# Kernel tuning notes

Hardware: AMD Instinct MI355X
Metric: run time of the kernel (lower is better)

## Reference

```python
import jax, jax.numpy as jnp
import numpy as np

B, L, D = 4, 2048, 2048
H, KVH, HD = 16, 4, 128          # num_heads, num_kv_heads, head_dim = D // H
M = 16                           # mem_tokens
BASE = 10000.0
EPS = 1.1920929e-07              # torch F.rms_norm default eps = fp32 machine eps


def _rms_norm(x):
    # normalize over last dim, no learned weight (matches F.rms_norm(x, (hd,)))
    return x * jax.lax.rsqrt(jnp.mean(x * x, axis=-1, keepdims=True) + EPS)


def _apply_rotary(x, cos, sin):
    # x: [B, h, T, HD]; cos/sin: [1, 1, T, HD//2]
    half = x.shape[-1] // 2
    x1, x2 = x[..., :half], x[..., half:]
    return jnp.concatenate([x1 * cos + x2 * sin, -x1 * sin + x2 * cos], axis=-1)


def setup_inputs() -> dict:
    key = jax.random.key(0)
    k0, k1, k2, k3, k4 = jax.random.split(key, 5)
    kv_dim = KVH * HD
    s = 0.02
    return {
        "x": jax.random.normal(k0, (B, L, D), dtype=jnp.float32),
        "Wq": jax.random.normal(k1, (D, D), dtype=jnp.float32) * s,
        "Wk": jax.random.normal(k2, (kv_dim, D), dtype=jnp.float32) * s,
        "Wv": jax.random.normal(k3, (kv_dim, D), dtype=jnp.float32) * s,
        "Wproj": jax.random.normal(k4, (D, D), dtype=jnp.float32) * s,
        "q_gain": jnp.full((H,), 1.0, dtype=jnp.float32),
    }


def reference(x, Wq, Wk, Wv, Wproj, q_gain):
    Bx, Lx, Dx = x.shape
    # QKV projections (Linear: x @ W.T), split into heads -> [B, h, L, HD]
    q = (x @ Wq.T).reshape(Bx, Lx, H, HD).transpose(0, 2, 1, 3)
    k = (x @ Wk.T).reshape(Bx, Lx, KVH, HD).transpose(0, 2, 1, 3)
    v = (x @ Wv.T).reshape(Bx, Lx, KVH, HD).transpose(0, 2, 1, 3)
    # QK RMSNorm
    q = _rms_norm(q)
    k = _rms_norm(k)
    # RoPE on the non-memory tokens only
    T = Lx - M
    inv_freq = 1.0 / BASE ** (jnp.arange(0, HD, 2, dtype=jnp.float32) / HD)
    freqs = jnp.outer(jnp.arange(T, dtype=jnp.float32), inv_freq)  # [T, HD//2]
    cos = jnp.cos(freqs)[None, None]
    sin = jnp.sin(freqs)[None, None]
    q = jnp.concatenate([q[:, :, :M], _apply_rotary(q[:, :, M:], cos, sin)], axis=2)
    k = jnp.concatenate([k[:, :, :M], _apply_rotary(k[:, :, M:], cos, sin)], axis=2)
    # per-head gain on q
    q = q * q_gain[None, :, None, None]
    # GQA attention: group q heads by kv head (matches repeat_interleave ordering)
    rep = H // KVH
    qg = q.reshape(Bx, KVH, rep, Lx, HD)
    scale = 1.0 / np.sqrt(HD).astype(np.float32)
    scores = jnp.einsum('bgrqd,bgkd->bgrqk', qg, k) * scale  # [B, KVH, rep, L, L]
    causal = jnp.tril(jnp.ones((Lx, Lx), dtype=bool))
    scores = jnp.where(causal, scores, -jnp.inf)
    p = jax.nn.softmax(scores, axis=-1)
    y = jnp.einsum('bgrqk,bgkd->bgrqd', p, v)                # [B, KVH, rep, L, HD]
    y = y.reshape(Bx, H, Lx, HD).transpose(0, 2, 1, 3).reshape(Bx, Lx, Dx)
    return y @ Wproj.T
```

## Files before the change

kernel.cpp:

```cpp
#include <hip/hip_runtime.h>
#include <stdint.h>

typedef unsigned short u16;
typedef short s8v __attribute__((ext_vector_type(8)));
typedef float f4v __attribute__((ext_vector_type(4)));
typedef float f16v __attribute__((ext_vector_type(16)));

typedef __attribute__((address_space(1))) char gchar;
typedef __attribute__((address_space(3))) char lchar;

static __device__ __forceinline__ u16 f2bf(float f) {
  uint32_t x = __float_as_uint(f);
  x += 0x7fffu + ((x >> 16) & 1u);
  return (u16)(x >> 16);
}
static __device__ __forceinline__ float bf2f(u16 u) {
  return __uint_as_float(((uint32_t)u) << 16);
}
static __device__ __forceinline__ void gload_lds16(const void* g, void* l) {
  __builtin_amdgcn_global_load_lds((gchar*)(uintptr_t)g,
                                   (lchar*)(uint32_t)(uintptr_t)l, 16, 0, 0);
}

__global__ __launch_bounds__(256) void cvt_bf16(const float4* __restrict__ src,
                                                uint2* __restrict__ dst, int n4) {
  int i = blockIdx.x * 256 + threadIdx.x;
  int st = gridDim.x * 256;
  for (; i < n4; i += st) {
    float4 v = src[i];
    uint2 o;
    o.x = (uint32_t)f2bf(v.x) | ((uint32_t)f2bf(v.y) << 16);
    o.y = (uint32_t)f2bf(v.z) | ((uint32_t)f2bf(v.w) << 16);
    dst[i] = o;
  }
}

__global__ __launch_bounds__(256) void cvt_bf16_w(const float4* __restrict__ s0,
                                                  const float4* __restrict__ s1,
                                                  const float4* __restrict__ s2,
                                                  const float4* __restrict__ s3,
                                                  uint2* __restrict__ dst) {
  int i = blockIdx.x * 256 + threadIdx.x;
  int st = gridDim.x * 256;
  for (; i < 2621440; i += st) {
    const float4* s;
    int off;
    if (i < 1048576)      { s = s0; off = i; }
    else if (i < 1310720) { s = s1; off = i - 1048576; }
    else if (i < 1572864) { s = s2; off = i - 1310720; }
    else                  { s = s3; off = i - 1572864; }
    float4 v = s[off];
    uint2 o;
    o.x = (uint32_t)f2bf(v.x) | ((uint32_t)f2bf(v.y) << 16);
    o.y = (uint32_t)f2bf(v.z) | ((uint32_t)f2bf(v.w) << 16);
    dst[i] = o;
  }
}

__global__ __launch_bounds__(256) void rope_table(float* __restrict__ tc,
                                                  float* __restrict__ ts) {
  int i = blockIdx.x * 256 + threadIdx.x;
  if (i >= 2032 * 64) return;
  int t = i >> 6, f = i & 63;
  float invf = 1.0f / powf(10000.0f, (float)f * (1.0f / 64.0f));
  float ang = (float)t * invf;
  float s, c;
  sincosf(ang, &s, &c);
  tc[i] = c;
  ts[i] = s;
}

template <int BN, int OUT>
__global__ __launch_bounds__(512, 2) void gemm_nt(
    const u16* __restrict__ A, const u16* __restrict__ Wt,
    u16* __restrict__ Oa, u16* __restrict__ Ob2, float* __restrict__ OF) {
  constexpr int MI = (BN == 256) ? 8 : 4;
  constexpr int BLOADS = (BN == 256) ? 2 : 1;
  __shared__ u16 lA[2][2][256 * 32];
  __shared__ u16 lB[2][2][BN * 32];
  const int tid = threadIdx.x;
  const int lane = tid & 63, wid = tid >> 6;
  const int wr = (BN == 256) ? (wid >> 2) : (wid >> 1);
  const int wc = (BN == 256) ? (wid & 3) : (wid & 1);
  const int l15 = lane & 15, l4 = lane >> 4;

  const int bid = blockIdx.x;
  const int swz = (bid & 7) * 32 + (bid >> 3);
  const int bn = swz >> 5, bm = swz & 31;
  const int m0 = bm * 256;
  const int n0r = bn * BN;

  auto stage_part = [&](int kt, int bs, int ks) {
    const int kb = kt * 64 + ks * 32;
#pragma unroll
    for (int c = 0; c < 2; ++c) {
      int cidx = tid + c * 512;
      int r = cidx >> 2, q = cidx & 3;
      int cc = q ^ ((r >> 2) & 3);
      gload_lds16(A + (size_t)(m0 + r) * 2048 + kb + cc * 8,
                  &lA[bs][ks][cidx * 8]);
    }
#pragma unroll
    for (int c = 0; c < BLOADS; ++c) {
      int cidx = tid + c * 512;
      int r = cidx >> 2, q = cidx & 3;
      int cc = q ^ ((r >> 2) & 3);
      gload_lds16(Wt + (size_t)(n0r + r) * 2048 + kb + cc * 8,
                  &lB[bs][ks][cidx * 8]);
    }
  };
  auto roff = [&](int fr, int c) {
    return (fr * 4 + (c ^ ((fr >> 2) & 3))) * 8;
  };

  const f4v Z4 = {0.f, 0.f, 0.f, 0.f};
  f4v acc[MI][4];
#pragma unroll
  for (int i = 0; i < MI; i++)
#pragma unroll
    for (int j = 0; j < 4; j++) acc[i][j] = Z4;

  stage_part(0, 0, 0); stage_part(0, 0, 1);
  stage_part(1, 1, 0); stage_part(1, 1, 1);

  const int NT = 32;
  for (int t = 0; t < NT; ++t) {
    const int bs = t & 1;
    if (t + 1 < NT) {
      if constexpr (BN == 256) asm volatile("s_waitcnt vmcnt(8)" ::: "memory");
      else                     asm volatile("s_waitcnt vmcnt(6)" ::: "memory");
    } else {
      asm volatile("s_waitcnt vmcnt(0)" ::: "memory");
    }
    asm volatile("s_barrier" ::: "memory");
    const bool pf = (t + 2 < NT);
#pragma unroll
    for (int ks = 0; ks < 2; ++ks) {
      s8v afrg[MI], bfrg[4];
#pragma unroll
      for (int i = 0; i < MI; ++i)
        afrg[i] = *(const s8v*)&lA[bs][ks][roff(wr * (MI * 16) + i * 16 + l15, l4)];
#pragma unroll
      for (int j = 0; j < 4; ++j)
        bfrg[j] = *(const s8v*)&lB[bs][ks][roff(wc * 64 + j * 16 + l15, l4)];
      asm volatile("s_waitcnt lgkmcnt(0)" ::: "memory");
      __builtin_amdgcn_sched_barrier(0);
      asm volatile("s_barrier" ::: "memory");
      if (pf) stage_part(t + 2, bs, ks);
      __builtin_amdgcn_s_setprio(1);
#pragma unroll
      for (int i = 0; i < MI; ++i)
#pragma unroll
        for (int j = 0; j < 4; ++j)
          acc[i][j] = __builtin_amdgcn_mfma_f32_16x16x32_bf16(afrg[i], bfrg[j], acc[i][j], 0, 0, 0);
      __builtin_amdgcn_s_setprio(0);
    }
  }

  const int colg = bn * BN + wc * 64;
  if constexpr (OUT == 0) {
    const int hh = colg >> 7, d0 = colg & 127;
#pragma unroll
    for (int i = 0; i < MI; i++)
#pragma unroll
      for (int r = 0; r < 4; r++) {
        int m = m0 + wr * (MI * 16) + i * 16 + l4 * 4 + r;
        int b = m >> 11, l = m & 2047;
        size_t base = ((size_t)(b * 16 + hh) * 2048 + l) * 128 + d0;
#pragma unroll
        for (int j = 0; j < 4; j++)
          Oa[base + j * 16 + l15] = f2bf(acc[i][j][r]);
      }
  } else if constexpr (OUT == 1) {
    u16* Ob = (colg < 512) ? Oa : Ob2;
    const int hh = (colg & 511) >> 7, d0 = colg & 127;
#pragma unroll
    for (int i = 0; i < MI; i++)
#pragma unroll
      for (int r = 0; r < 4; r++) {
        int m = m0 + wr * (MI * 16) + i * 16 + l4 * 4 + r;
        int b = m >> 11, l = m & 2047;
        size_t base = ((size_t)(b * 4 + hh) * 2048 + l) * 128 + d0;
#pragma unroll
        for (int j = 0; j < 4; j++)
          Ob[base + j * 16 + l15] = f2bf(acc[i][j][r]);
      }
  } else {
#pragma unroll
    for (int i = 0; i < MI; i++)
#pragma unroll
      for (int r = 0; r < 4; r++) {
        int m = m0 + wr * (MI * 16) + i * 16 + l4 * 4 + r;
#pragma unroll
        for (int j = 0; j < 4; j++)
          OF[(size_t)m * 2048 + colg + j * 16 + l15] = acc[i][j][r];
      }
  }
}

__global__ __launch_bounds__(256) void norm_rope(u16* __restrict__ buf,
                                                 const float* __restrict__ gain,
                                                 const float* __restrict__ tc,
                                                 const float* __restrict__ ts) {
  const int lane = threadIdx.x & 63;
  const int gw = blockIdx.x * 4 + (threadIdx.x >> 6);
  const int nw = gridDim.x * 4;
  for (int row = gw; row < 163840; row += nw) {
    int l = row & 2047;
    u16* p = buf + (size_t)row * 128;
    float x1 = bf2f(p[lane]);
    float x2 = bf2f(p[lane + 64]);
    float ss = x1 * x1 + x2 * x2;
#pragma unroll
    for (int off = 32; off > 0; off >>= 1) ss += __shfl_xor(ss, off, 64);
    float r = rsqrtf(ss * (1.0f / 128.0f) + 1.1920929e-07f);
    x1 *= r; x2 *= r;
    if (l >= 16) {
      int t = l - 16;
      float c = tc[t * 64 + lane], s = ts[t * 64 + lane];
      float o1 = x1 * c + x2 * s;
      float o2 = -x1 * s + x2 * c;
      x1 = o1; x2 = o2;
    }
    if (row < 131072) {
      float g = gain[(row >> 11) & 15] *
                (0.08838834764831845f * 1.4426950408889634f);
      x1 *= g; x2 *= g;
    }
    p[lane] = f2bf(x1);
    p[lane + 64] = f2bf(x2);
  }
}

__global__ __launch_bounds__(256) void transpose_v(const u16* __restrict__ v,
                                                   u16* __restrict__ vt) {
  __shared__ u16 t[64][64];
  const int l0 = blockIdx.x * 64, d0 = blockIdx.y * 64, bg = blockIdx.z;
  const int tid = threadIdx.x;
#pragma unroll
  for (int it = 0; it < 2; ++it) {
    int lin = it * 256 + tid;
    int r = lin >> 3, cb = lin & 7;
    s8v val = *(const s8v*)&v[((bg * 2048 + l0 + r) * 128) + d0 + cb * 8];
    *(s8v*)&t[r][(cb ^ (r & 7)) * 8] = val;
  }
  __syncthreads();
#pragma unroll
  for (int it = 0; it < 2; ++it) {
    int lin = it * 256 + tid;
    int r2 = lin >> 3, c2 = (lin & 7) * 8;
    s8v o;
#pragma unroll
    for (int j = 0; j < 8; ++j) {
      int rr = c2 + j, cc = r2;
      o[j] = (short)t[rr][(cc & 7) + 8 * ((cc >> 3) ^ (rr & 7))];
    }
    *(s8v*)&vt[((bg * 128 + d0 + r2) * 2048) + l0 + c2] = o;
  }
}

__global__ __launch_bounds__(256, 2) void attn(const u16* __restrict__ q,
                                               const u16* __restrict__ k,
                                               const u16* __restrict__ vt,
                                               u16* __restrict__ y) {
  __shared__ u16 lK[2][64 * 128];
  __shared__ u16 lVT[2][128 * 64];
  const int tid = threadIdx.x;
  const int lane = tid & 63, wid = tid >> 6;
  const int l31 = lane & 31, hi = lane >> 5;

  const int db = (int)blockIdx.y * 32 + (int)blockIdx.x;
  const int half = db >> 8, rem = db & 255;
  const int bg = (rem & 7) + 8 * half;
  const int pairi = rem >> 3;
  const int b = bg >> 2, g = bg & 3;
  const int h = g * 4 + wid;

  const u16* qh = q + (size_t)(b * 16 + h) * 2048 * 128;
  const u16* kb0 = k + (size_t)(b * 4 + g) * 2048 * 128;
  const u16* vtb0 = vt + (size_t)(b * 4 + g) * 128 * 2048;

  auto stage = [&](int t, int bufsel) {
    const int kv0 = t * 64;
#pragma unroll
    for (int it = 0; it < 4; ++it) {
      int lin = it * 256 + tid;
      int kj = lin >> 4, s = lin & 15;
      gload_lds16(kb0 + (size_t)(kv0 + kj) * 128 + ((s ^ (kj & 7)) * 8),
                  &lK[bufsel][lin * 8]);
    }
#pragma unroll
    for (int it = 0; it < 4; ++it) {
      int lin = it * 256 + tid;
      int d = lin >> 3, s = lin & 7;
      gload_lds16(vtb0 + (size_t)d * 2048 + kv0 + ((s ^ (d & 7)) * 8),
                  &lVT[bufsel][lin * 8]);
    }
  };

  for (int ph = 0; ph < 2; ++ph) {
    const int qt = ph ? (63 - pairi) : pairi;
    const int q0 = qt * 32;
    const int nt = (q0 >> 6) + 1;
    const int qabs = q0 + l31;

    s8v qf[8];
#pragma unroll
    for (int ks = 0; ks < 8; ++ks)
      qf[ks] = *(const s8v*)&qh[(q0 + l31) * 128 + ks * 16 + hi * 8];

    f16v yacc[4];
#pragma unroll
    for (int j = 0; j < 4; ++j)
#pragma unroll
      for (int r = 0; r < 16; ++r) yacc[j][r] = 0.f;
    float mrow = -1e30f, lrow = 0.f;

    stage(0, 0);
    __syncthreads();

    for (int t = 0; t < nt; ++t) {
      const int cur = t & 1;
      if (t + 1 < nt) stage(t + 1, cur ^ 1);
      const int kv0 = t * 64;

      f16v s0a, s1a;
#pragma unroll
      for (int r = 0; r < 16; ++r) { s0a[r] = 0.f; s1a[r] = 0.f; }
      __builtin_amdgcn_s_setprio(1);
#pragma unroll
      for (int ks = 0; ks < 8; ++ks) {
        const int slot = (2 * ks + hi) ^ (l31 & 7);
        s8v kf0 = *(const s8v*)&lK[cur][(l31)*128 + slot * 8];
        s8v kf1 = *(const s8v*)&lK[cur][(32 + l31) * 128 + slot * 8];
        s0a = __builtin_amdgcn_mfma_f32_32x32x16_bf16(kf0, qf[ks], s0a, 0, 0, 0);
        s1a = __builtin_amdgcn_mfma_f32_32x32x16_bf16(kf1, qf[ks], s1a, 0, 0, 0);
      }
      __builtin_amdgcn_s_setprio(0);

      const bool last = (t == nt - 1);
      float p0[16], p1[16];
      float pmax = -1e30f;
#pragma unroll
      for (int r = 0; r < 16; ++r) {
        const int kvloc = (r & 3) + 8 * (r >> 2) + 4 * hi;
        float v0 = s0a[r];
        float v1 = s1a[r];
        if (last) {
          if (kv0 + kvloc > qabs) v0 = -1e30f;
          if (kv0 + 32 + kvloc > qabs) v1 = -1e30f;
        }
        p0[r] = v0; p1[r] = v1;
        pmax = fmaxf(pmax, fmaxf(v0, v1));
      }
      pmax = fmaxf(pmax, __shfl_xor(pmax, 32, 64));

      if (!__all(pmax - mrow <= 11.541560327111707f)) {
        float mnew = fmaxf(mrow, pmax);
        float corr = __builtin_amdgcn_exp2f(mrow - mnew);
#pragma unroll
        for (int r = 0; r < 16; ++r) {
          const int qloc = (r & 3) + 8 * (r >> 2) + 4 * hi;
          float cb = __shfl(corr, qloc, 64);
          yacc[0][r] *= cb; yacc[1][r] *= cb; yacc[2][r] *= cb; yacc[3][r] *= cb;
        }
        lrow *= corr;
        mrow = mnew;
      }

      float ps = 0.f;
#pragma unroll
      for (int r = 0; r < 16; ++r) {
        float e0 = __builtin_amdgcn_exp2f(p0[r] - mrow);
        float e1 = __builtin_amdgcn_exp2f(p1[r] - mrow);
        p0[r] = e0; p1[r] = e1;
        ps += e0 + e1;
      }
      ps += __shfl_xor(ps, 32, 64);
      lrow += ps;

      __builtin_amdgcn_s_setprio(1);
#pragma unroll
      for (int ks = 0; ks < 4; ++ks) {
        const float* pc = (ks < 2) ? p0 : p1;
        const int rb = 8 * (ks & 1);
        uint32_t A0, A1, B0, B1;
        asm("v_cvt_pk_bf16_f32 %0, %1, %2" : "=v"(A0) : "v"(pc[rb + 0]), "v"(pc[rb + 1]));
        asm("v_cvt_pk_bf16_f32 %0, %1, %2" : "=v"(A1) : "v"(pc[rb + 2]), "v"(pc[rb + 3]));
        asm("v_cvt_pk_bf16_f32 %0, %1, %2" : "=v"(B0) : "v"(pc[rb + 4]), "v"(pc[rb + 5]));
        asm("v_cvt_pk_bf16_f32 %0, %1, %2" : "=v"(B1) : "v"(pc[rb + 6]), "v"(pc[rb + 7]));
        uint32_t t0 = hi ? A0 : B0;
        uint32_t t1 = hi ? A1 : B1;
        uint32_t r0 = (uint32_t)__shfl_xor((int)t0, 32, 64);
        uint32_t r1 = (uint32_t)__shfl_xor((int)t1, 32, 64);
        union { uint32_t u[4]; s8v v; } uu;
        uu.u[0] = hi ? r0 : A0;
        uu.u[1] = hi ? r1 : A1;
        uu.u[2] = hi ? B0 : r0;
        uu.u[3] = hi ? B1 : r1;
#pragma unroll
        for (int jd = 0; jd < 4; ++jd) {
          const int rowd = 32 * jd + l31;
          const int slot = (2 * ks + hi) ^ (l31 & 7);
          s8v vf = *(const s8v*)&lVT[cur][rowd * 64 + slot * 8];
          yacc[jd] = __builtin_amdgcn_mfma_f32_32x32x16_bf16(uu.v, vf, yacc[jd], 0, 0, 0);
        }
      }
      __builtin_amdgcn_s_setprio(0);
      __syncthreads();
    }

    float inv = 1.0f / lrow;
#pragma unroll
    for (int r = 0; r < 16; ++r) {
      const int qloc = (r & 3) + 8 * (r >> 2) + 4 * hi;
      float ib = __shfl(inv, qloc, 64);
      const int qrow = q0 + qloc;
      size_t base = ((size_t)(b * 2048 + qrow)) * 2048 + h * 128 + l31;
#pragma unroll
      for (int jd = 0; jd < 4; ++jd)
        y[base + 32 * jd] = f2bf(yacc[jd][r] * ib);
    }
  }
}

extern "C" void kernel_launch(void* const* d_in, const int* in_sizes, int n_in,
                              void* d_out, int out_size, void* d_ws, size_t ws_size,
                              hipStream_t stream) {
  const float* x  = (const float*)d_in[0];
  const float* Wq = (const float*)d_in[1];
  const float* Wk = (const float*)d_in[2];
  const float* Wv = (const float*)d_in[3];
  const float* Wp = (const float*)d_in[4];
  const float* qg = (const float*)d_in[5];
  float* out = (float*)d_out;

  char* ws = (char*)d_ws;
  size_t off = 0;
  auto alloc = [&](size_t bytes) {
    void* p = ws + off;
    off += (bytes + 255) & ~(size_t)255;
    return p;
  };
  u16* x_bf  = (u16*)alloc((size_t)8192 * 2048 * 2);
  u16* wq_bf = (u16*)alloc((size_t)2048 * 2048 * 2);
  u16* wk_bf = (u16*)alloc((size_t)512 * 2048 * 2);
  u16* wv_bf = (u16*)alloc((size_t)512 * 2048 * 2);
  u16* wp_bf = (u16*)alloc((size_t)2048 * 2048 * 2);
  u16* q_bf  = (u16*)alloc((size_t)4 * 16 * 2048 * 128 * 2);
  u16* k_bf  = (u16*)alloc((size_t)4 * 4 * 2048 * 128 * 2);
  u16* v_bf  = (u16*)alloc((size_t)4 * 4 * 2048 * 128 * 2);
  float* tab = (float*)alloc((size_t)2032 * 64 * 2 * 4);
  u16* y_bf  = x_bf;
  u16* vt_bf = wq_bf;

  cvt_bf16<<<2048, 256, 0, stream>>>((const float4*)x, (uint2*)x_bf, 8192 * 2048 / 4);
  cvt_bf16_w<<<1024, 256, 0, stream>>>((const float4*)Wq, (const float4*)Wk,
                                       (const float4*)Wv, (const float4*)Wp,
                                       (uint2*)wq_bf);
  rope_table<<<(2032 * 64 + 255) / 256, 256, 0, stream>>>(tab, tab + 2032 * 64);

  gemm_nt<256, 0><<<dim3(256), 512, 0, stream>>>(x_bf, wq_bf, q_bf, nullptr, nullptr);
  gemm_nt<128, 1><<<dim3(256), 512, 0, stream>>>(x_bf, wk_bf, k_bf, v_bf, nullptr);
  norm_rope<<<2048, 256, 0, stream>>>(q_bf, qg, tab, tab + 2032 * 64);
  transpose_v<<<dim3(32, 2, 16), 256, 0, stream>>>(v_bf, vt_bf);
  attn<<<dim3(32, 16), 256, 0, stream>>>(q_bf, k_bf, vt_bf, y_bf);
  gemm_nt<256, 2><<<dim3(256), 512, 0, stream>>>(y_bf, wp_bf, nullptr, nullptr, out);
}
```

Measured before the change: 357.1 us.

## Fuse Q RMSNorm/RoPE/gain into attention and widen blocks to 512 threads

The Q normalization, rotary embedding and gain scaling move into the attention kernel's Q-fragment load, so the separate norm pass now handles only K and the Q buffer is no longer read and rewritten. The attention kernel switches from a 256-thread block processing two paired 32-row Q tiles in sequence to a 512-thread block processing one 64-row Q tile, with two wave sets sharing each K/V stage. The lane-swap shuffle is replaced by v_permlane32_swap. This trades the causal load balance of paired tiles, since blocks now have uneven work, and adds register pressure under launch_bounds(512,2).

```diff
diff --git a/kernel.cpp b/kernel.cpp
--- a/kernel.cpp
+++ b/kernel.cpp
@@ -198,14 +198,13 @@
   }
 }
 
-__global__ __launch_bounds__(256) void norm_rope(u16* __restrict__ buf,
-                                                 const float* __restrict__ gain,
-                                                 const float* __restrict__ tc,
-                                                 const float* __restrict__ ts) {
+__global__ __launch_bounds__(256) void norm_rope_k(u16* __restrict__ buf,
+                                                   const float* __restrict__ tc,
+                                                   const float* __restrict__ ts) {
   const int lane = threadIdx.x & 63;
   const int gw = blockIdx.x * 4 + (threadIdx.x >> 6);
   const int nw = gridDim.x * 4;
-  for (int row = gw; row < 163840; row += nw) {
+  for (int row = gw; row < 32768; row += nw) {
     int l = row & 2047;
     u16* p = buf + (size_t)row * 128;
     float x1 = bf2f(p[lane]);
@@ -222,11 +221,6 @@
       float o2 = -x1 * s + x2 * c;
       x1 = o1; x2 = o2;
     }
-    if (row < 131072) {
-      float g = gain[(row >> 11) & 15] *
-                (0.08838834764831845f * 1.4426950408889634f);
-      x1 *= g; x2 *= g;
-    }
     p[lane] = f2bf(x1);
     p[lane + 64] = f2bf(x2);
   }
@@ -259,10 +253,13 @@
   }
 }
 
-__global__ __launch_bounds__(256, 2) void attn(const u16* __restrict__ q,
+__global__ __launch_bounds__(512, 2) void attn(const u16* __restrict__ q,
                                                const u16* __restrict__ k,
                                                const u16* __restrict__ vt,
-                                               u16* __restrict__ y) {
+                                               u16* __restrict__ y,
+                                               const float* __restrict__ qg,
+                                               const float* __restrict__ tc,
+                                               const float* __restrict__ ts) {
   __shared__ u16 lK[2][64 * 128];
   __shared__ u16 lVT[2][128 * 64];
   const int tid = threadIdx.x;
@@ -272,155 +269,198 @@
   const int db = (int)blockIdx.y * 32 + (int)blockIdx.x;
   const int half = db >> 8, rem = db & 255;
   const int bg = (rem & 7) + 8 * half;
-  const int pairi = rem >> 3;
+  const int qi = rem >> 3;
+  const int qt = 31 - qi;
   const int b = bg >> 2, g = bg & 3;
-  const int h = g * 4 + wid;
+  const int h = g * 4 + (wid & 3);
+  const int se = wid >> 2;
+  const int q0 = qt * 64;
+  const int nt = qt + 1;
 
   const u16* qh = q + (size_t)(b * 16 + h) * 2048 * 128;
   const u16* kb0 = k + (size_t)(b * 4 + g) * 2048 * 128;
   const u16* vtb0 = vt + (size_t)(b * 4 + g) * 128 * 2048;
 
+  const int pos = q0 + 32 * se + l31;
+  const float gscale = qg[h] * (0.08838834764831845f * 1.4426950408889634f);
+  s8v qf[8];
+  {
+    const u16* qp = qh + (size_t)pos * 128 + hi * 8;
+    s8v qr[8];
+#pragma unroll
+    for (int ks = 0; ks < 8; ++ks) qr[ks] = *(const s8v*)&qp[ks * 16];
+    float ssum = 0.f;
+#pragma unroll
+    for (int ks = 0; ks < 8; ++ks)
+#pragma unroll
+      for (int j = 0; j < 8; ++j) {
+        float v = bf2f((u16)qr[ks][j]);
+        ssum += v * v;
+      }
+    ssum += __shfl_xor(ssum, 32, 64);
+    const float rn = rsqrtf(ssum * (1.0f / 128.0f) + 1.1920929e-07f) * gscale;
+    const bool rot = (pos >= 16);
+    const int tt = pos - 16;
+#pragma unroll
+    for (int ks = 0; ks < 4; ++ks) {
+      float cv[8], sv[8];
+      if (rot) {
+        const float* cp = &tc[tt * 64 + ks * 16 + hi * 8];
+        const float* sp = &ts[tt * 64 + ks * 16 + hi * 8];
+        *(float4*)&cv[0] = *(const float4*)cp;
+        *(float4*)&cv[4] = *(const float4*)(cp + 4);
+        *(float4*)&sv[0] = *(const float4*)sp;
+        *(float4*)&sv[4] = *(const float4*)(sp + 4);
+      }
+      uint32_t wlo[4], whi[4];
+#pragma unroll
+      for (int j2 = 0; j2 < 4; ++j2) {
+        float o1[2], o2[2];
+#pragma unroll
+        for (int e = 0; e < 2; ++e) {
+          const int j = j2 * 2 + e;
+          float x1 = bf2f((u16)qr[ks][j]);
+          float x2 = bf2f((u16)qr[ks + 4][j]);
+          float a = x1, bb = x2;
+          if (rot) { a = x1 * cv[j] + x2 * sv[j]; bb = x2 * cv[j] - x1 * sv[j]; }
+          o1[e] = a * rn;
+          o2[e] = bb * rn;
+        }
+        asm("v_cvt_pk_bf16_f32 %0, %1, %2" : "=v"(wlo[j2]) : "v"(o1[0]), "v"(o1[1]));
+        asm("v_cvt_pk_bf16_f32 %0, %1, %2" : "=v"(whi[j2]) : "v"(o2[0]), "v"(o2[1]));
+      }
+      union { uint32_t u[4]; s8v v; } ua, ub;
+      ua.u[0] = wlo[0]; ua.u[1] = wlo[1]; ua.u[2] = wlo[2]; ua.u[3] = wlo[3];
+      ub.u[0] = whi[0]; ub.u[1] = whi[1]; ub.u[2] = whi[2]; ub.u[3] = whi[3];
+      qf[ks] = ua.v;
+      qf[ks + 4] = ub.v;
+    }
+  }
+
   auto stage = [&](int t, int bufsel) {
     const int kv0 = t * 64;
 #pragma unroll
-    for (int it = 0; it < 4; ++it) {
-      int lin = it * 256 + tid;
+    for (int it = 0; it < 2; ++it) {
+      int lin = it * 512 + tid;
       int kj = lin >> 4, s = lin & 15;
       gload_lds16(kb0 + (size_t)(kv0 + kj) * 128 + ((s ^ (kj & 7)) * 8),
                   &lK[bufsel][lin * 8]);
     }
 #pragma unroll
-    for (int it = 0; it < 4; ++it) {
-      int lin = it * 256 + tid;
+    for (int it = 0; it < 2; ++it) {
+      int lin = it * 512 + tid;
       int d = lin >> 3, s = lin & 7;
       gload_lds16(vtb0 + (size_t)d * 2048 + kv0 + ((s ^ (d & 7)) * 8),
                   &lVT[bufsel][lin * 8]);
     }
   };
 
-  for (int ph = 0; ph < 2; ++ph) {
-    const int qt = ph ? (63 - pairi) : pairi;
-    const int q0 = qt * 32;
-    const int nt = (q0 >> 6) + 1;
-    const int qabs = q0 + l31;
-
-    s8v qf[8];
-#pragma unroll
-    for (int ks = 0; ks < 8; ++ks)
-      qf[ks] = *(const s8v*)&qh[(q0 + l31) * 128 + ks * 16 + hi * 8];
-
-    f16v yacc[4];
-#pragma unroll
-    for (int j = 0; j < 4; ++j)
-#pragma unroll
-      for (int r = 0; r < 16; ++r) yacc[j][r] = 0.f;
-    float mrow = -1e30f, lrow = 0.f;
-
-    stage(0, 0);
+  f16v yacc[4];
+#pragma unroll
+  for (int j = 0; j < 4; ++j)
+#pragma unroll
+    for (int r = 0; r < 16; ++r) yacc[j][r] = 0.f;
+  float mrow = -1e30f, lrow = 0.f;
+
+  stage(0, 0);
+  __syncthreads();
+
+  for (int t = 0; t < nt; ++t) {
+    const int cur = t & 1;
+    if (t + 1 < nt) stage(t + 1, cur ^ 1);
+    const int kv0 = t * 64;
+
+    f16v s0a, s1a;
+#pragma unroll
+    for (int r = 0; r < 16; ++r) { s0a[r] = 0.f; s1a[r] = 0.f; }
+    __builtin_amdgcn_s_setprio(1);
+#pragma unroll
+    for (int ks = 0; ks < 8; ++ks) {
+      const int slot = (2 * ks + hi) ^ (l31 & 7);
+      s8v kf0 = *(const s8v*)&lK[cur][(l31)*128 + slot * 8];
+      s8v kf1 = *(const s8v*)&lK[cur][(32 + l31) * 128 + slot * 8];
+      s0a = __builtin_amdgcn_mfma_f32_32x32x16_bf16(kf0, qf[ks], s0a, 0, 0, 0);
+      s1a = __builtin_amdgcn_mfma_f32_32x32x16_bf16(kf1, qf[ks], s1a, 0, 0, 0);
+    }
+    __builtin_amdgcn_s_setprio(0);
+
+    const bool last = (t == nt - 1);
+    float p0[16], p1[16];
+    float pmax = -1e30f;
+#pragma unroll
+    for (int r = 0; r < 16; ++r) {
+      const int kvloc = (r & 3) + 8 * (r >> 2) + 4 * hi;
+      float v0 = s0a[r];
+      float v1 = s1a[r];
+      if (last) {
+        if (kv0 + kvloc > pos) v0 = -1e30f;
+        if (kv0 + 32 + kvloc > pos) v1 = -1e30f;
+      }
+      p0[r] = v0; p1[r] = v1;
+      pmax = fmaxf(pmax, fmaxf(v0, v1));
+    }
+    pmax = fmaxf(pmax, __shfl_xor(pmax, 32, 64));
+
+    if (!__all(pmax - mrow <= 11.541560327111707f)) {
+      float mnew = fmaxf(mrow, pmax);
+      float corr = __builtin_amdgcn_exp2f(mrow - mnew);
+#pragma unroll
+      for (int r = 0; r < 16; ++r) {
+        const int qloc = (r & 3) + 8 * (r >> 2) + 4 * hi;
+        float cb = __shfl(corr, qloc, 64);
+        yacc[0][r] *= cb; yacc[1][r] *= cb; yacc[2][r] *= cb; yacc[3][r] *= cb;
+      }
+      lrow *= corr;
+      mrow = mnew;
+    }
+
+    float ps = 0.f;
+#pragma unroll
+    for (int r = 0; r < 16; ++r) {
+      float e0 = __builtin_amdgcn_exp2f(p0[r] - mrow);
+      float e1 = __builtin_amdgcn_exp2f(p1[r] - mrow);
+      p0[r] = e0; p1[r] = e1;
+      ps += e0 + e1;
+    }
+    ps += __shfl_xor(ps, 32, 64);
+    lrow += ps;
+
+    __builtin_amdgcn_s_setprio(1);
+#pragma unroll
+    for (int ks = 0; ks < 4; ++ks) {
+      const float* pc = (ks < 2) ? p0 : p1;
+      const int rb = 8 * (ks & 1);
+      uint32_t A0, A1, B0, B1;
+      asm("v_cvt_pk_bf16_f32 %0, %1, %2" : "=v"(A0) : "v"(pc[rb + 0]), "v"(pc[rb + 1]));
+      asm("v_cvt_pk_bf16_f32 %0, %1, %2" : "=v"(A1) : "v"(pc[rb + 2]), "v"(pc[rb + 3]));
+      asm("v_cvt_pk_bf16_f32 %0, %1, %2" : "=v"(B0) : "v"(pc[rb + 4]), "v"(pc[rb + 5]));
+      asm("v_cvt_pk_bf16_f32 %0, %1, %2" : "=v"(B1) : "v"(pc[rb + 6]), "v"(pc[rb + 7]));
+      asm("v_permlane32_swap_b32 %0, %1" : "+v"(A0), "+v"(B0));
+      asm("v_permlane32_swap_b32 %0, %1" : "+v"(A1), "+v"(B1));
+      union { uint32_t u[4]; s8v v; } uu;
+      uu.u[0] = A0; uu.u[1] = A1; uu.u[2] = B0; uu.u[3] = B1;
+#pragma unroll
+      for (int jd = 0; jd < 4; ++jd) {
+        const int rowd = 32 * jd + l31;
+        const int slot = (2 * ks + hi) ^ (l31 & 7);
+        s8v vf = *(const s8v*)&lVT[cur][rowd * 64 + slot * 8];
+        yacc[jd] = __builtin_amdgcn_mfma_f32_32x32x16_bf16(uu.v, vf, yacc[jd], 0, 0, 0);
+      }
+    }
+    __builtin_amdgcn_s_setprio(0);
     __syncthreads();
-
-    for (int t = 0; t < nt; ++t) {
-      const int cur = t & 1;
-      if (t + 1 < nt) stage(t + 1, cur ^ 1);
-      const int kv0 = t * 64;
-
-      f16v s0a, s1a;
-#pragma unroll
-      for (int r = 0; r < 16; ++r) { s0a[r] = 0.f; s1a[r] = 0.f; }
-      __builtin_amdgcn_s_setprio(1);
-#pragma unroll
-      for (int ks = 0; ks < 8; ++ks) {
-        const int slot = (2 * ks + hi) ^ (l31 & 7);
-        s8v kf0 = *(const s8v*)&lK[cur][(l31)*128 + slot * 8];
-        s8v kf1 = *(const s8v*)&lK[cur][(32 + l31) * 128 + slot * 8];
-        s0a = __builtin_amdgcn_mfma_f32_32x32x16_bf16(kf0, qf[ks], s0a, 0, 0, 0);
-        s1a = __builtin_amdgcn_mfma_f32_32x32x16_bf16(kf1, qf[ks], s1a, 0, 0, 0);
-      }
-      __builtin_amdgcn_s_setprio(0);
-
-      const bool last = (t == nt - 1);
-      float p0[16], p1[16];
-      float pmax = -1e30f;
-#pragma unroll
-      for (int r = 0; r < 16; ++r) {
-        const int kvloc = (r & 3) + 8 * (r >> 2) + 4 * hi;
-        float v0 = s0a[r];
-        float v1 = s1a[r];
-        if (last) {
-          if (kv0 + kvloc > qabs) v0 = -1e30f;
-          if (kv0 + 32 + kvloc > qabs) v1 = -1e30f;
-        }
-        p0[r] = v0; p1[r] = v1;
-        pmax = fmaxf(pmax, fmaxf(v0, v1));
-      }
-      pmax = fmaxf(pmax, __shfl_xor(pmax, 32, 64));
-
-      if (!__all(pmax - mrow <= 11.541560327111707f)) {
-        float mnew = fmaxf(mrow, pmax);
-        float corr = __builtin_amdgcn_exp2f(mrow - mnew);
-#pragma unroll
-        for (int r = 0; r < 16; ++r) {
-          const int qloc = (r & 3) + 8 * (r >> 2) + 4 * hi;
-          float cb = __shfl(corr, qloc, 64);
-          yacc[0][r] *= cb; yacc[1][r] *= cb; yacc[2][r] *= cb; yacc[3][r] *= cb;
-        }
-        lrow *= corr;
-        mrow = mnew;
-      }
-
-      float ps = 0.f;
-#pragma unroll
-      for (int r = 0; r < 16; ++r) {
-        float e0 = __builtin_amdgcn_exp2f(p0[r] - mrow);
-        float e1 = __builtin_amdgcn_exp2f(p1[r] - mrow);
-        p0[r] = e0; p1[r] = e1;
-        ps += e0 + e1;
-      }
-      ps += __shfl_xor(ps, 32, 64);
-      lrow += ps;
-
-      __builtin_amdgcn_s_setprio(1);
-#pragma unroll
-      for (int ks = 0; ks < 4; ++ks) {
-        const float* pc = (ks < 2) ? p0 : p1;
-        const int rb = 8 * (ks & 1);
-        uint32_t A0, A1, B0, B1;
-        asm("v_cvt_pk_bf16_f32 %0, %1, %2" : "=v"(A0) : "v"(pc[rb + 0]), "v"(pc[rb + 1]));
-        asm("v_cvt_pk_bf16_f32 %0, %1, %2" : "=v"(A1) : "v"(pc[rb + 2]), "v"(pc[rb + 3]));
-        asm("v_cvt_pk_bf16_f32 %0, %1, %2" : "=v"(B0) : "v"(pc[rb + 4]), "v"(pc[rb + 5]));
-        asm("v_cvt_pk_bf16_f32 %0, %1, %2" : "=v"(B1) : "v"(pc[rb + 6]), "v"(pc[rb + 7]));
-        uint32_t t0 = hi ? A0 : B0;
-        uint32_t t1 = hi ? A1 : B1;
-        uint32_t r0 = (uint32_t)__shfl_xor((int)t0, 32, 64);
-        uint32_t r1 = (uint32_t)__shfl_xor((int)t1, 32, 64);
-        union { uint32_t u[4]; s8v v; } uu;
-        uu.u[0] = hi ? r0 : A0;
-        uu.u[1] = hi ? r1 : A1;
-        uu.u[2] = hi ? B0 : r0;
-        uu.u[3] = hi ? B1 : r1;
-#pragma unroll
-        for (int jd = 0; jd < 4; ++jd) {
-          const int rowd = 32 * jd + l31;
-          const int slot = (2 * ks + hi) ^ (l31 & 7);
-          s8v vf = *(const s8v*)&lVT[cur][rowd * 64 + slot * 8];
-          yacc[jd] = __builtin_amdgcn_mfma_f32_32x32x16_bf16(uu.v, vf, yacc[jd], 0, 0, 0);
-        }
-      }
-      __builtin_amdgcn_s_setprio(0);
-      __syncthreads();
-    }
-
-    float inv = 1.0f / lrow;
-#pragma unroll
-    for (int r = 0; r < 16; ++r) {
-      const int qloc = (r & 3) + 8 * (r >> 2) + 4 * hi;
-      float ib = __shfl(inv, qloc, 64);
-      const int qrow = q0 + qloc;
-      size_t base = ((size_t)(b * 2048 + qrow)) * 2048 + h * 128 + l31;
-#pragma unroll
-      for (int jd = 0; jd < 4; ++jd)
-        y[base + 32 * jd] = f2bf(yacc[jd][r] * ib);
-    }
+  }
+
+  float inv = 1.0f / lrow;
+#pragma unroll
+  for (int r = 0; r < 16; ++r) {
+    const int qloc = (r & 3) + 8 * (r >> 2) + 4 * hi;
+    float ib = __shfl(inv, qloc, 64);
+    const int qrow = q0 + 32 * se + qloc;
+    size_t base = ((size_t)(b * 2048 + qrow)) * 2048 + h * 128 + l31;
+#pragma unroll
+    for (int jd = 0; jd < 4; ++jd)
+      y[base + 32 * jd] = f2bf(yacc[jd][r] * ib);
   }
 }
 
@@ -462,8 +502,9 @@
 
   gemm_nt<256, 0><<<dim3(256), 512, 0, stream>>>(x_bf, wq_bf, q_bf, nullptr, nullptr);
   gemm_nt<128, 1><<<dim3(256), 512, 0, stream>>>(x_bf, wk_bf, k_bf, v_bf, nullptr);
-  norm_rope<<<2048, 256, 0, stream>>>(q_bf, qg, tab, tab + 2032 * 64);
+  norm_rope_k<<<256, 256, 0, stream>>>(k_bf, tab, tab + 2032 * 64);
   transpose_v<<<dim3(32, 2, 16), 256, 0, stream>>>(v_bf, vt_bf);
-  attn<<<dim3(32, 16), 256, 0, stream>>>(q_bf, k_bf, vt_bf, y_bf);
+  attn<<<dim3(32, 16), 512, 0, stream>>>(q_bf, k_bf, vt_bf, y_bf, qg,
+                                         tab, tab + 2032 * 64);
   gemm_nt<256, 2><<<dim3(256), 512, 0, stream>>>(y_bf, wp_bf, nullptr, nullptr, out);
 }
```

After: 374.4 us. 1.05x slower.
